# Kernel optimization log

Hardware: AMD Instinct MI355X
Metric: run time of the kernel (lower is better)

## Reference

```python
import jax, jax.numpy as jnp
import numpy as np

SPATIAL_SHAPES = ((128, 128), (64, 64), (32, 32), (16, 16))  # (h, w) per level
N_HEADS, N_LEVELS, N_POINTS, D_MODEL = 8, 4, 4, 256


def setup_inputs() -> dict:
    key = jax.random.key(0)
    ks = jax.random.split(key, 10)
    bs, nq, nk = 4, 300, 17
    inp = {
        'query': jax.random.normal(ks[0], (bs, nq * nk, D_MODEL), jnp.float32),
        'reference_points': jax.random.uniform(ks[1], (bs, nq, N_LEVELS, nk, 2), jnp.float32),
    }
    for l, (h, w) in enumerate(SPATIAL_SHAPES):
        inp[f'value{l}'] = jax.random.normal(ks[2 + l], (bs * N_HEADS, D_MODEL // N_HEADS, h * w), jnp.float32)
    inp['W_off'] = jax.random.normal(ks[6], (N_HEADS * N_LEVELS * N_POINTS * 2, D_MODEL), jnp.float32) * 0.02
    inp['b_off'] = jax.random.normal(ks[7], (N_HEADS * N_LEVELS * N_POINTS * 2,), jnp.float32) * 0.5
    inp['W_attn'] = jax.random.normal(ks[8], (N_HEADS * N_LEVELS * N_POINTS, D_MODEL), jnp.float32) * 0.02
    inp['b_attn'] = jax.random.normal(ks[9], (N_HEADS * N_LEVELS * N_POINTS,), jnp.float32) * 0.02
    return inp


def _bilinear_sample(v, grid, h, w):
    # v: (N, C, h*w); grid: (N, P, 2) normalized to [-1, 1] (x, y).
    # F.grid_sample bilinear, padding_mode='zeros', align_corners=False.
    x = (grid[..., 0] + 1.0) * 0.5 * w - 0.5
    y = (grid[..., 1] + 1.0) * 0.5 * h - 0.5
    x0 = jnp.floor(x)
    y0 = jnp.floor(y)
    wx1, wy1 = x - x0, y - y0
    wx0, wy0 = 1.0 - wx1, 1.0 - wy1
    x0i, y0i = x0.astype(jnp.int32), y0.astype(jnp.int32)
    out = 0.0
    for xi, yi, wgt in ((x0i, y0i, wx0 * wy0), (x0i + 1, y0i, wx1 * wy0),
                        (x0i, y0i + 1, wx0 * wy1), (x0i + 1, y0i + 1, wx1 * wy1)):
        valid = (xi >= 0) & (xi < w) & (yi >= 0) & (yi < h)
        idx = jnp.clip(yi, 0, h - 1) * w + jnp.clip(xi, 0, w - 1)       # (N, P)
        g = jnp.take_along_axis(v, idx[:, None, :], axis=2)              # (N, C, P)
        out = out + g * (wgt * valid.astype(v.dtype))[:, None, :]
    return out


def reference(query, reference_points, value0, value1, value2, value3, W_off, b_off, W_attn, b_attn):
    bs, len_q, _ = query.shape
    hd = D_MODEL // N_HEADS
    values = (value0, value1, value2, value3)

    off = (query @ W_off.T + b_off).reshape(bs, len_q, N_HEADS, N_LEVELS, N_POINTS, 2)
    attn = (query @ W_attn.T + b_attn).reshape(bs, len_q, N_HEADS, N_LEVELS * N_POINTS)
    attn = jax.nn.softmax(attn, axis=-1)

    # (bs, nq, L, nk, 2) -> transpose(2,3) -> flatten(1,2) -> (bs, len_q, L, 2)
    rp = jnp.transpose(reference_points, (0, 1, 3, 2, 4)).reshape(bs, len_q, N_LEVELS, 2)
    # normalizer: spatial (h, w) flipped -> (w, h)
    norm = jnp.array([[w, h] for (h, w) in SPATIAL_SHAPES], dtype=query.dtype).reshape(1, 1, 1, N_LEVELS, 1, 2)
    loc = rp[:, :, None, :, None, :] + off / norm                         # (bs, len_q, H, L, P, 2)

    grids = 2.0 * loc - 1.0
    grids = jnp.transpose(grids, (0, 2, 1, 3, 4, 5)).reshape(bs * N_HEADS, len_q, N_LEVELS, N_POINTS, 2)

    sampled = []
    for l, (h, w) in enumerate(SPATIAL_SHAPES):
        g = grids[:, :, l].reshape(bs * N_HEADS, len_q * N_POINTS, 2)
        s = _bilinear_sample(values[l], g, h, w)                          # (bs*H, hd, len_q*P)
        sampled.append(s.reshape(bs * N_HEADS, hd, len_q, N_POINTS))
    sampled = jnp.concatenate(sampled, axis=-1)                           # (bs*H, hd, len_q, L*P)

    attn_r = jnp.transpose(attn, (0, 2, 1, 3)).reshape(bs * N_HEADS, 1, len_q, N_LEVELS * N_POINTS)
    out = (sampled * attn_r).sum(-1).reshape(bs, D_MODEL, len_q)
    return jnp.transpose(out, (0, 2, 1))                                  # (bs, len_q, d_model)
```

## Files before the change

### kernel.cpp

```cpp
#include <hip/hip_runtime.h>
#include <math.h>

#define BS        4
#define NQ        300
#define NK        17
#define LEN_Q     5100
#define N_HEADS   8
#define N_LEVELS  4
#define N_POINTS  4
#define D_MODEL   256
#define HD        32

#define LB0 0
#define LB1 16777216
#define LB2 20971520
#define LB3 22020096
#define VT_TOTAL 22282240

typedef __attribute__((ext_vector_type(8))) short bf16x8;
typedef __attribute__((ext_vector_type(4))) float f32x4;

__device__ __forceinline__ unsigned short f2bf(float x) {
    unsigned u = __float_as_uint(x);
    unsigned r = (u + 0x7fffu + ((u >> 16) & 1u)) >> 16;
    return (unsigned short)r;
}
__device__ __forceinline__ float bf2f(unsigned short s) {
    return __uint_as_float((unsigned)s << 16);
}
__device__ __forceinline__ bf16x8 cvt8(const float* __restrict__ p) {
    float4 a = *(const float4*)p;
    float4 b = *(const float4*)(p + 4);
    bf16x8 r;
    r[0] = f2bf(a.x); r[1] = f2bf(a.y); r[2] = f2bf(a.z); r[3] = f2bf(a.w);
    r[4] = f2bf(b.x); r[5] = f2bf(b.y); r[6] = f2bf(b.z); r[7] = f2bf(b.w);
    return r;
}

__global__ __launch_bounds__(256) void transpose_bf16_kernel(
    const float* __restrict__ v0, const float* __restrict__ v1,
    const float* __restrict__ v2, const float* __restrict__ v3,
    unsigned short* __restrict__ vt)
{
    __shared__ float t[32][33];
    int bx = blockIdx.x;
    int n  = blockIdx.y;

    const float* in; int S; size_t ob; int tile;
    if (bx < 512)      { in = v0; S = 16384; ob = LB0; tile = bx; }
    else if (bx < 640) { in = v1; S = 4096;  ob = LB1; tile = bx - 512; }
    else if (bx < 672) { in = v2; S = 1024;  ob = LB2; tile = bx - 640; }
    else               { in = v3; S = 256;   ob = LB3; tile = bx - 672; }

    int s0 = tile * 32;
    const float* pin = in + (size_t)n * 32 * S;
    #pragma unroll
    for (int c = threadIdx.y; c < 32; c += 8) {
        t[c][threadIdx.x] = pin[(size_t)c * S + s0 + threadIdx.x];
    }
    __syncthreads();
    unsigned short* pout = vt + ob + (size_t)n * S * 32;
    #pragma unroll
    for (int r = threadIdx.y; r < 32; r += 8) {
        pout[(size_t)(s0 + r) * 32 + threadIdx.x] = f2bf(t[threadIdx.x][r]);
    }
}

__global__ __launch_bounds__(256) void proj_gemm_mfma(
    const float* __restrict__ Q,
    const float* __restrict__ Woff, const float* __restrict__ boff,
    const float* __restrict__ Wattn, const float* __restrict__ battn,
    float* __restrict__ P, int M)
{
    int tid  = threadIdx.x;
    int wave = tid >> 6;
    int lane = tid & 63;
    int bm = blockIdx.y * 64;
    int bn = blockIdx.x * 128;
    int wm = (wave & 1) * 32;
    int wn = (wave >> 1) * 64;
    int lr = lane & 15;
    int lk = (lane >> 4) * 8;

    f32x4 acc[2][4] = {};
    for (int k0 = 0; k0 < 256; k0 += 32) {
        bf16x8 afrag[2], bfrag[4];
        #pragma unroll
        for (int i = 0; i < 2; ++i) {
            int row = bm + wm + i * 16 + lr;
            row = row < M ? row : M - 1;
            afrag[i] = cvt8(Q + (size_t)row * 256 + k0 + lk);
        }
        #pragma unroll
        for (int j = 0; j < 4; ++j) {
            int n = bn + wn + j * 16 + lr;
            const float* wp = (n < 256) ? (Woff + (size_t)n * 256)
                                        : (Wattn + (size_t)(n - 256) * 256);
            bfrag[j] = cvt8(wp + k0 + lk);
        }
        #pragma unroll
        for (int i = 0; i < 2; ++i)
            #pragma unroll
            for (int j = 0; j < 4; ++j)
                acc[i][j] = __builtin_amdgcn_mfma_f32_16x16x32_bf16(
                    afrag[i], bfrag[j], acc[i][j], 0, 0, 0);
    }

    #pragma unroll
    for (int i = 0; i < 2; ++i) {
        int mbase = bm + wm + i * 16 + (lane >> 4) * 4;
        #pragma unroll
        for (int j = 0; j < 4; ++j) {
            int n = bn + wn + j * 16 + (lane & 15);
            float bias = (n < 256) ? boff[n] : battn[n - 256];
            #pragma unroll
            for (int r = 0; r < 4; ++r) {
                int row = mbase + r;
                if (row < M) P[(size_t)row * 384 + n] = acc[i][j][r] + bias;
            }
        }
    }
}

__global__ __launch_bounds__(256) void ms_deform_kernel(
    const float* __restrict__ rp,
    const float* __restrict__ proj,
    const unsigned short* __restrict__ vt,
    float* __restrict__ out)
{
    int bid = blockIdx.x;
    int h   = bid & 7;
    int b   = (bid >> 3) & 3;
    int qc  = bid >> 5;
    int q0  = qc * 8;

    __shared__ int s_iw[1552];
    __shared__ float4 s_red[256];

    int tid = threadIdx.x;

    if (tid < 128) {
        int q8 = tid >> 4;
        int lp = tid & 15;
        int l  = lp >> 2;
        int p  = lp & 3;
        int q  = q0 + q8;
        int qq = q < LEN_Q ? q : LEN_Q - 1;
        const float* prow = proj + (size_t)(b * LEN_Q + qq) * 384;

        float g = prow[256 + h * 16 + lp];
        float mx = g;
        mx = fmaxf(mx, __shfl_xor(mx, 1, 16));
        mx = fmaxf(mx, __shfl_xor(mx, 2, 16));
        mx = fmaxf(mx, __shfl_xor(mx, 4, 16));
        mx = fmaxf(mx, __shfl_xor(mx, 8, 16));
        float e = __expf(g - mx);
        float s = e;
        s += __shfl_xor(s, 1, 16);
        s += __shfl_xor(s, 2, 16);
        s += __shfl_xor(s, 4, 16);
        s += __shfl_xor(s, 8, 16);
        float a = (q < LEN_Q) ? (e / s) : 0.f;

        int Wl = 128 >> l;
        float ww = (float)Wl;
        int qi = qq / NK;
        int ki = qq - qi * NK;
        size_t rbase = ((((size_t)b * NQ + qi) * N_LEVELS + l) * NK + ki) * 2;
        float rx = rp[rbase + 0];
        float ry = rp[rbase + 1];
        int oj = (h * 16 + lp) * 2;
        float ox = prow[oj], oy = prow[oj + 1];
        float x = (rx + ox / ww) * ww - 0.5f;
        float y = (ry + oy / ww) * ww - 0.5f;
        float x0f = floorf(x), y0f = floorf(y);
        float wx1 = x - x0f, wy1 = y - y0f;
        float wx0 = 1.f - wx1, wy0 = 1.f - wy1;
        int x0 = (int)x0f, y0 = (int)y0f;

        int* wrow = s_iw + (q8 >> 1) * 388 + (p * 8 + l * 2 + (q8 & 1)) * 12;
        #pragma unroll
        for (int corner = 0; corner < 4; ++corner) {
            int xi = x0 + (corner & 1);
            int yi = y0 + (corner >> 1);
            float wgt = ((corner & 1) ? wx1 : wx0) * ((corner >> 1) ? wy1 : wy0);
            bool valid = (xi >= 0) && (xi < Wl) && (yi >= 0) && (yi < Wl);
            int2 iw;
            iw.x = valid ? (yi * Wl + xi) * HD : 0;
            iw.y = __float_as_int(valid ? wgt * a : 0.f);
            *(int2*)(wrow + corner * 2) = iw;
        }
    }
    __syncthreads();

    int l  = tid >> 6;
    int q8 = (tid >> 3) & 7;
    int c4 = tid & 7;
    int n  = b * N_HEADS + h;
    const size_t lb[4]  = {LB0, LB1, LB2, LB3};
    const int    Ssz[4] = {16384, 4096, 1024, 256};

    const unsigned short* vbase = vt + lb[l] + (size_t)n * Ssz[l] * HD + c4 * 4;
    const int* rrow0 = s_iw + (q8 >> 1) * 388 + (l * 2 + (q8 & 1)) * 12;

    float4 acc = make_float4(0.f, 0.f, 0.f, 0.f);
    #pragma unroll
    for (int p = 0; p < 4; ++p) {
        const int* rr = rrow0 + p * 96;
        int4 A  = *(const int4*)rr;
        int4 Bv = *(const int4*)(rr + 4);
        ushort4 u0 = *(const ushort4*)(vbase + A.x);
        ushort4 u1 = *(const ushort4*)(vbase + A.z);
        ushort4 u2 = *(const ushort4*)(vbase + Bv.x);
        ushort4 u3 = *(const ushort4*)(vbase + Bv.z);
        float w0 = __int_as_float(A.y);
        float w1 = __int_as_float(A.w);
        float w2 = __int_as_float(Bv.y);
        float w3 = __int_as_float(Bv.w);
        acc.x += w0 * bf2f(u0.x) + w1 * bf2f(u1.x) + w2 * bf2f(u2.x) + w3 * bf2f(u3.x);
        acc.y += w0 * bf2f(u0.y) + w1 * bf2f(u1.y) + w2 * bf2f(u2.y) + w3 * bf2f(u3.y);
        acc.z += w0 * bf2f(u0.z) + w1 * bf2f(u1.z) + w2 * bf2f(u2.z) + w3 * bf2f(u3.z);
        acc.w += w0 * bf2f(u0.w) + w1 * bf2f(u1.w) + w2 * bf2f(u2.w) + w3 * bf2f(u3.w);
    }

    s_red[tid] = acc;
    __syncthreads();
    if (tid < 64) {
        int q8o = tid >> 3;
        int c4o = tid & 7;
        int base = q8o * 8 + c4o;
        float4 a0 = s_red[base];
        float4 a1 = s_red[base + 64];
        float4 a2 = s_red[base + 128];
        float4 a3 = s_red[base + 192];
        float4 o;
        o.x = a0.x + a1.x + a2.x + a3.x;
        o.y = a0.y + a1.y + a2.y + a3.y;
        o.z = a0.z + a1.z + a2.z + a3.z;
        o.w = a0.w + a1.w + a2.w + a3.w;
        int q = q0 + q8o;
        if (q < LEN_Q)
            *(float4*)(out + (size_t)(b * LEN_Q + q) * 256 + h * 32 + c4o * 4) = o;
    }
}

extern "C" void kernel_launch(void* const* d_in, const int* in_sizes, int n_in,
                              void* d_out, int out_size, void* d_ws, size_t ws_size,
                              hipStream_t stream)
{
    const float* query = (const float*)d_in[0];
    const float* refp  = (const float*)d_in[1];
    const float* v0    = (const float*)d_in[2];
    const float* v1    = (const float*)d_in[3];
    const float* v2    = (const float*)d_in[4];
    const float* v3    = (const float*)d_in[5];
    const float* Woff  = (const float*)d_in[6];
    const float* boff  = (const float*)d_in[7];
    const float* Wattn = (const float*)d_in[8];
    const float* battn = (const float*)d_in[9];
    float* out = (float*)d_out;
    unsigned short* vt = (unsigned short*)d_ws;
    float* proj = (float*)(vt + VT_TOTAL);

    transpose_bf16_kernel<<<dim3(680, 32), dim3(32, 8), 0, stream>>>(
        v0, v1, v2, v3, vt);

    int M = BS * LEN_Q;
    proj_gemm_mfma<<<dim3(3, (M + 63) / 64), 256, 0, stream>>>(
        query, Woff, boff, Wattn, battn, proj, M);

    ms_deform_kernel<<<638 * 32, 256, 0, stream>>>(refp, proj, vt, out);
}
```

Before: 129.1 us.

## Merge transpose and projection GEMM into one launch; widen sampler to 16 queries

The value transpose/bf16 conversion and the projection GEMM now run as one kernel, with each block choosing its role by block index. This saves a launch and lets the two independent stages overlap on the GPU. The sampling kernel now handles 16 queries per block with all 256 threads computing sampling weights, and each thread loads 8 bf16 channels instead of 4, halving the block count. The cost is more shared memory per block, and an 8-wide gather still reads only 16 bytes per corner.

```diff
diff --git a/kernel.cpp b/kernel.cpp
--- a/kernel.cpp
+++ b/kernel.cpp
@@ -17,7 +17,11 @@
 #define LB3 22020096
 #define VT_TOTAL 22282240
 
+#define NGEMM 957
+#define NTRANS 21760
+
 typedef __attribute__((ext_vector_type(8))) short bf16x8;
+typedef __attribute__((ext_vector_type(8))) unsigned short ushort8_t;
 typedef __attribute__((ext_vector_type(4))) float f32x4;
 
 __device__ __forceinline__ unsigned short f2bf(float x) {
@@ -37,87 +41,88 @@
     return r;
 }
 
-__global__ __launch_bounds__(256) void transpose_bf16_kernel(
-    const float* __restrict__ v0, const float* __restrict__ v1,
-    const float* __restrict__ v2, const float* __restrict__ v3,
-    unsigned short* __restrict__ vt)
-{
-    __shared__ float t[32][33];
-    int bx = blockIdx.x;
-    int n  = blockIdx.y;
-
-    const float* in; int S; size_t ob; int tile;
-    if (bx < 512)      { in = v0; S = 16384; ob = LB0; tile = bx; }
-    else if (bx < 640) { in = v1; S = 4096;  ob = LB1; tile = bx - 512; }
-    else if (bx < 672) { in = v2; S = 1024;  ob = LB2; tile = bx - 640; }
-    else               { in = v3; S = 256;   ob = LB3; tile = bx - 672; }
-
-    int s0 = tile * 32;
-    const float* pin = in + (size_t)n * 32 * S;
-    #pragma unroll
-    for (int c = threadIdx.y; c < 32; c += 8) {
-        t[c][threadIdx.x] = pin[(size_t)c * S + s0 + threadIdx.x];
-    }
-    __syncthreads();
-    unsigned short* pout = vt + ob + (size_t)n * S * 32;
-    #pragma unroll
-    for (int r = threadIdx.y; r < 32; r += 8) {
-        pout[(size_t)(s0 + r) * 32 + threadIdx.x] = f2bf(t[threadIdx.x][r]);
-    }
-}
-
-__global__ __launch_bounds__(256) void proj_gemm_mfma(
+__global__ __launch_bounds__(256) void prep_kernel(
     const float* __restrict__ Q,
     const float* __restrict__ Woff, const float* __restrict__ boff,
     const float* __restrict__ Wattn, const float* __restrict__ battn,
-    float* __restrict__ P, int M)
+    const float* __restrict__ v0, const float* __restrict__ v1,
+    const float* __restrict__ v2, const float* __restrict__ v3,
+    unsigned short* __restrict__ vt, float* __restrict__ P, int M)
 {
-    int tid  = threadIdx.x;
-    int wave = tid >> 6;
-    int lane = tid & 63;
-    int bm = blockIdx.y * 64;
-    int bn = blockIdx.x * 128;
-    int wm = (wave & 1) * 32;
-    int wn = (wave >> 1) * 64;
-    int lr = lane & 15;
-    int lk = (lane >> 4) * 8;
-
-    f32x4 acc[2][4] = {};
-    for (int k0 = 0; k0 < 256; k0 += 32) {
-        bf16x8 afrag[2], bfrag[4];
+    __shared__ float t[32][33];
+    int bid = blockIdx.x;
+    int tid = threadIdx.x;
+
+    if (bid < NGEMM) {
+        int wave = tid >> 6;
+        int lane = tid & 63;
+        int bm = (bid / 3) * 64;
+        int bn = (bid % 3) * 128;
+        int wm = (wave & 1) * 32;
+        int wn = (wave >> 1) * 64;
+        int lr = lane & 15;
+        int lk = (lane >> 4) * 8;
+
+        f32x4 acc[2][4] = {};
+        for (int k0 = 0; k0 < 256; k0 += 32) {
+            bf16x8 afrag[2], bfrag[4];
+            #pragma unroll
+            for (int i = 0; i < 2; ++i) {
+                int row = bm + wm + i * 16 + lr;
+                row = row < M ? row : M - 1;
+                afrag[i] = cvt8(Q + (size_t)row * 256 + k0 + lk);
+            }
+            #pragma unroll
+            for (int j = 0; j < 4; ++j) {
+                int n = bn + wn + j * 16 + lr;
+                const float* wp = (n < 256) ? (Woff + (size_t)n * 256)
+                                            : (Wattn + (size_t)(n - 256) * 256);
+                bfrag[j] = cvt8(wp + k0 + lk);
+            }
+            #pragma unroll
+            for (int i = 0; i < 2; ++i)
+                #pragma unroll
+                for (int j = 0; j < 4; ++j)
+                    acc[i][j] = __builtin_amdgcn_mfma_f32_16x16x32_bf16(
+                        afrag[i], bfrag[j], acc[i][j], 0, 0, 0);
+        }
         #pragma unroll
         for (int i = 0; i < 2; ++i) {
-            int row = bm + wm + i * 16 + lr;
-            row = row < M ? row : M - 1;
-            afrag[i] = cvt8(Q + (size_t)row * 256 + k0 + lk);
-        }
-        #pragma unroll
-        for (int j = 0; j < 4; ++j) {
-            int n = bn + wn + j * 16 + lr;
-            const float* wp = (n < 256) ? (Woff + (size_t)n * 256)
-                                        : (Wattn + (size_t)(n - 256) * 256);
-            bfrag[j] = cvt8(wp + k0 + lk);
-        }
-        #pragma unroll
-        for (int i = 0; i < 2; ++i)
-            #pragma unroll
-            for (int j = 0; j < 4; ++j)
-                acc[i][j] = __builtin_amdgcn_mfma_f32_16x16x32_bf16(
-                    afrag[i], bfrag[j], acc[i][j], 0, 0, 0);
-    }
-
-    #pragma unroll
-    for (int i = 0; i < 2; ++i) {
-        int mbase = bm + wm + i * 16 + (lane >> 4) * 4;
-        #pragma unroll
-        for (int j = 0; j < 4; ++j) {
-            int n = bn + wn + j * 16 + (lane & 15);
-            float bias = (n < 256) ? boff[n] : battn[n - 256];
-            #pragma unroll
-            for (int r = 0; r < 4; ++r) {
-                int row = mbase + r;
-                if (row < M) P[(size_t)row * 384 + n] = acc[i][j][r] + bias;
+            int mbase = bm + wm + i * 16 + (lane >> 4) * 4;
+            #pragma unroll
+            for (int j = 0; j < 4; ++j) {
+                int n = bn + wn + j * 16 + (lane & 15);
+                float bias = (n < 256) ? boff[n] : battn[n - 256];
+                #pragma unroll
+                for (int r = 0; r < 4; ++r) {
+                    int row = mbase + r;
+                    if (row < M) P[(size_t)row * 384 + n] = acc[i][j][r] + bias;
+                }
             }
+        }
+    } else {
+        int tb = bid - NGEMM;
+        int bx = tb % 680;
+        int n  = tb / 680;
+        const float* in; int S; size_t ob; int tile;
+        if (bx < 512)      { in = v0; S = 16384; ob = LB0; tile = bx; }
+        else if (bx < 640) { in = v1; S = 4096;  ob = LB1; tile = bx - 512; }
+        else if (bx < 672) { in = v2; S = 1024;  ob = LB2; tile = bx - 640; }
+        else               { in = v3; S = 256;   ob = LB3; tile = bx - 672; }
+
+        int tx = tid & 31;
+        int ty = tid >> 5;
+        int s0 = tile * 32;
+        const float* pin = in + (size_t)n * 32 * S;
+        #pragma unroll
+        for (int c = ty; c < 32; c += 8) {
+            t[c][tx] = pin[(size_t)c * S + s0 + tx];
+        }
+        __syncthreads();
+        unsigned short* pout = vt + ob + (size_t)n * S * 32;
+        #pragma unroll
+        for (int r = ty; r < 32; r += 8) {
+            pout[(size_t)(s0 + r) * 32 + tx] = f2bf(t[tx][r]);
         }
     }
 }
@@ -132,19 +137,19 @@
     int h   = bid & 7;
     int b   = (bid >> 3) & 3;
     int qc  = bid >> 5;
-    int q0  = qc * 8;
-
-    __shared__ int s_iw[1552];
-    __shared__ float4 s_red[256];
+    int q0  = qc * 16;
+
+    __shared__ int s_iw[3104];
+    __shared__ float4 s_red4[2][256];
 
     int tid = threadIdx.x;
 
-    if (tid < 128) {
-        int q8 = tid >> 4;
+    {
+        int qL = tid >> 4;
         int lp = tid & 15;
         int l  = lp >> 2;
         int p  = lp & 3;
-        int q  = q0 + q8;
+        int q  = q0 + qL;
         int qq = q < LEN_Q ? q : LEN_Q - 1;
         const float* prow = proj + (size_t)(b * LEN_Q + qq) * 384;
 
@@ -178,7 +183,7 @@
         float wx0 = 1.f - wx1, wy0 = 1.f - wy1;
         int x0 = (int)x0f, y0 = (int)y0f;
 
-        int* wrow = s_iw + (q8 >> 1) * 388 + (p * 8 + l * 2 + (q8 & 1)) * 12;
+        int* wrow = s_iw + (qL >> 1) * 388 + (p * 8 + l * 2 + (qL & 1)) * 12;
         #pragma unroll
         for (int corner = 0; corner < 4; ++corner) {
             int xi = x0 + (corner & 1);
@@ -194,53 +199,60 @@
     __syncthreads();
 
     int l  = tid >> 6;
-    int q8 = (tid >> 3) & 7;
-    int c4 = tid & 7;
+    int qL = (tid >> 2) & 15;
+    int c8 = tid & 3;
     int n  = b * N_HEADS + h;
     const size_t lb[4]  = {LB0, LB1, LB2, LB3};
     const int    Ssz[4] = {16384, 4096, 1024, 256};
 
-    const unsigned short* vbase = vt + lb[l] + (size_t)n * Ssz[l] * HD + c4 * 4;
-    const int* rrow0 = s_iw + (q8 >> 1) * 388 + (l * 2 + (q8 & 1)) * 12;
-
-    float4 acc = make_float4(0.f, 0.f, 0.f, 0.f);
+    const unsigned short* vbase = vt + lb[l] + (size_t)n * Ssz[l] * HD + c8 * 8;
+    const int* rrow0 = s_iw + (qL >> 1) * 388 + (l * 2 + (qL & 1)) * 12;
+
+    float4 accA = make_float4(0.f, 0.f, 0.f, 0.f);
+    float4 accB = make_float4(0.f, 0.f, 0.f, 0.f);
     #pragma unroll
     for (int p = 0; p < 4; ++p) {
         const int* rr = rrow0 + p * 96;
         int4 A  = *(const int4*)rr;
         int4 Bv = *(const int4*)(rr + 4);
-        ushort4 u0 = *(const ushort4*)(vbase + A.x);
-        ushort4 u1 = *(const ushort4*)(vbase + A.z);
-        ushort4 u2 = *(const ushort4*)(vbase + Bv.x);
-        ushort4 u3 = *(const ushort4*)(vbase + Bv.z);
+        ushort8_t u0 = *(const ushort8_t*)(vbase + A.x);
+        ushort8_t u1 = *(const ushort8_t*)(vbase + A.z);
+        ushort8_t u2 = *(const ushort8_t*)(vbase + Bv.x);
+        ushort8_t u3 = *(const ushort8_t*)(vbase + Bv.z);
         float w0 = __int_as_float(A.y);
         float w1 = __int_as_float(A.w);
         float w2 = __int_as_float(Bv.y);
         float w3 = __int_as_float(Bv.w);
-        acc.x += w0 * bf2f(u0.x) + w1 * bf2f(u1.x) + w2 * bf2f(u2.x) + w3 * bf2f(u3.x);
-        acc.y += w0 * bf2f(u0.y) + w1 * bf2f(u1.y) + w2 * bf2f(u2.y) + w3 * bf2f(u3.y);
-        acc.z += w0 * bf2f(u0.z) + w1 * bf2f(u1.z) + w2 * bf2f(u2.z) + w3 * bf2f(u3.z);
-        acc.w += w0 * bf2f(u0.w) + w1 * bf2f(u1.w) + w2 * bf2f(u2.w) + w3 * bf2f(u3.w);
-    }
-
-    s_red[tid] = acc;
+        accA.x += w0 * bf2f(u0[0]) + w1 * bf2f(u1[0]) + w2 * bf2f(u2[0]) + w3 * bf2f(u3[0]);
+        accA.y += w0 * bf2f(u0[1]) + w1 * bf2f(u1[1]) + w2 * bf2f(u2[1]) + w3 * bf2f(u3[1]);
+        accA.z += w0 * bf2f(u0[2]) + w1 * bf2f(u1[2]) + w2 * bf2f(u2[2]) + w3 * bf2f(u3[2]);
+        accA.w += w0 * bf2f(u0[3]) + w1 * bf2f(u1[3]) + w2 * bf2f(u2[3]) + w3 * bf2f(u3[3]);
+        accB.x += w0 * bf2f(u0[4]) + w1 * bf2f(u1[4]) + w2 * bf2f(u2[4]) + w3 * bf2f(u3[4]);
+        accB.y += w0 * bf2f(u0[5]) + w1 * bf2f(u1[5]) + w2 * bf2f(u2[5]) + w3 * bf2f(u3[5]);
+        accB.z += w0 * bf2f(u0[6]) + w1 * bf2f(u1[6]) + w2 * bf2f(u2[6]) + w3 * bf2f(u3[6]);
+        accB.w += w0 * bf2f(u0[7]) + w1 * bf2f(u1[7]) + w2 * bf2f(u2[7]) + w3 * bf2f(u3[7]);
+    }
+
+    s_red4[0][tid] = accA;
+    s_red4[1][tid] = accB;
     __syncthreads();
-    if (tid < 64) {
-        int q8o = tid >> 3;
-        int c4o = tid & 7;
-        int base = q8o * 8 + c4o;
-        float4 a0 = s_red[base];
-        float4 a1 = s_red[base + 64];
-        float4 a2 = s_red[base + 128];
-        float4 a3 = s_red[base + 192];
+    if (tid < 128) {
+        int qo = tid >> 3;
+        int co = (tid >> 1) & 3;
+        int hf = tid & 1;
+        int base = qo * 4 + co;
+        float4 a0 = s_red4[hf][base];
+        float4 a1 = s_red4[hf][base + 64];
+        float4 a2 = s_red4[hf][base + 128];
+        float4 a3 = s_red4[hf][base + 192];
         float4 o;
         o.x = a0.x + a1.x + a2.x + a3.x;
         o.y = a0.y + a1.y + a2.y + a3.y;
         o.z = a0.z + a1.z + a2.z + a3.z;
         o.w = a0.w + a1.w + a2.w + a3.w;
-        int q = q0 + q8o;
+        int q = q0 + qo;
         if (q < LEN_Q)
-            *(float4*)(out + (size_t)(b * LEN_Q + q) * 256 + h * 32 + c4o * 4) = o;
+            *(float4*)(out + (size_t)(b * LEN_Q + q) * 256 + h * 32 + co * 8 + hf * 4) = o;
     }
 }
 
@@ -262,12 +274,10 @@
     unsigned short* vt = (unsigned short*)d_ws;
     float* proj = (float*)(vt + VT_TOTAL);
 
-    transpose_bf16_kernel<<<dim3(680, 32), dim3(32, 8), 0, stream>>>(
-        v0, v1, v2, v3, vt);
-
     int M = BS * LEN_Q;
-    proj_gemm_mfma<<<dim3(3, (M + 63) / 64), 256, 0, stream>>>(
-        query, Woff, boff, Wattn, battn, proj, M);
-
-    ms_deform_kernel<<<638 * 32, 256, 0, stream>>>(refp, proj, vt, out);
-}
+
+    prep_kernel<<<NGEMM + NTRANS, 256, 0, stream>>>(
+        query, Woff, boff, Wattn, battn, v0, v1, v2, v3, vt, proj, M);
+
+    ms_deform_kernel<<<319 * 32, 256, 0, stream>>>(refp, proj, vt, out);
+}
```

After: 142.2 us. +10.1%, slower.
